# Performance work log

Hardware: AMD Instinct MI355X
Metric: run time of the kernel (lower is better)

Reference implementation:

```python
import jax, jax.numpy as jnp
import numpy as np

B, N, N_IN, MSG_HID, MSG_OUT, N_HID, N_OUT, K = 32, 128, 16, 64, 64, 64, 16, 4
E = N * (N - 1)  # 16256 directed edges, fully connected w/o self-loops


def setup_inputs() -> dict:
    key = jax.random.key(0)
    ks = jax.random.split(key, 8)
    # one-hot relation matrices (NRI convention)
    rows, cols = np.where(np.ones((N, N)) - np.eye(N))
    eye = np.eye(N, dtype=np.float32)
    rel_rec = jnp.asarray(eye[rows])   # [E, N]
    rel_send = jnp.asarray(eye[cols])  # [E, N]
    s = 0.1  # weight init scale
    return {
        "inputs": jax.random.normal(ks[0], (B, N_IN, N), jnp.float32),
        "rel_rec": rel_rec,
        "rel_send": rel_send,
        "rel_types": jax.nn.softmax(jax.random.normal(ks[1], (B, E, K), jnp.float32), axis=-1),
        "W1": jax.random.normal(ks[2], (K, 2 * N_IN, MSG_HID), jnp.float32) * s,
        "b1": jnp.zeros((K, MSG_HID), jnp.float32),
        "W2": jax.random.normal(ks[3], (K, MSG_HID, MSG_OUT), jnp.float32) * s,
        "b2": jnp.zeros((K, MSG_OUT), jnp.float32),
        "Wo1": jax.random.normal(ks[4], (MSG_OUT + N_IN, N_HID), jnp.float32) * s,
        "bo1": jnp.zeros((N_HID,), jnp.float32),
        "Wo2": jax.random.normal(ks[5], (N_HID, N_HID), jnp.float32) * s,
        "bo2": jnp.zeros((N_HID,), jnp.float32),
        "Wo3": jax.random.normal(ks[6], (N_HID, N_OUT), jnp.float32) * s,
        "bo3": jnp.zeros((N_OUT,), jnp.float32),
    }


def reference(inputs, rel_rec, rel_send, rel_types, W1, b1, W2, b2, Wo1, bo1, Wo2, bo2, Wo3, bo3):
    x = jnp.transpose(inputs, (0, 2, 1))                     # [B, N, n_in]
    senders = jnp.einsum('en,bnf->bef', rel_send, x)          # [B, E, n_in]
    receivers = jnp.einsum('en,bnf->bef', rel_rec, x)         # [B, E, n_in]
    pre_msg = jnp.concatenate([senders, receivers], axis=-1)  # [B, E, 2*n_in]
    all_msgs = jnp.zeros((pre_msg.shape[0], pre_msg.shape[1], W2.shape[-1]), pre_msg.dtype)
    for k in range(W1.shape[0]):  # small fixed loop over edge types
        m = jax.nn.relu(pre_msg @ W1[k] + b1[k])
        m = jax.nn.relu(m @ W2[k] + b2[k])
        all_msgs = all_msgs + m * rel_types[:, :, k:k + 1]
    # edge2node aggregation (no normalization in forward path, matches source)
    agg_msgs = jnp.einsum('bem,en->bnm', all_msgs, rel_rec)   # [B, N, msg_out]
    aug_msgs = jnp.concatenate([x, agg_msgs], axis=-1)        # [B, N, n_in+msg_out]
    h = jax.nn.relu(aug_msgs @ Wo1 + bo1)  # dropout disabled (eval mode)
    h = jax.nn.relu(h @ Wo2 + bo2)
    pred = h @ Wo3 + bo3                                      # [B, N, n_out]
    return jnp.transpose(pred, (0, 2, 1))                     # [B, n_out, N]
```

## Files before the change

kernel.cpp:

```cpp
#include <hip/hip_runtime.h>
#include <stdint.h>

#define B_  32
#define N_  128
#define NIN 16
#define K_  4
#define E_  (N_*(N_-1))

typedef float    f4 __attribute__((ext_vector_type(4)));
typedef _Float16 h8 __attribute__((ext_vector_type(8)));
typedef _Float16 h4 __attribute__((ext_vector_type(4)));

__global__ __launch_bounds__(256) void prep(
    const float* __restrict__ inp, const float* __restrict__ W1,
    const float* __restrict__ b1,  const float* __restrict__ W2,
    const float* __restrict__ Wo1, const float* __restrict__ Wo2,
    const float* __restrict__ Wo3, const float* __restrict__ rt,
    _Float16* __restrict__ Sh, _Float16* __restrict__ Rh,
    _Float16* __restrict__ w2h, _Float16* __restrict__ wn,
    _Float16* __restrict__ rtn)
{
    const int bid = blockIdx.x;
    const int tid = threadIdx.x;
    if (bid < 1024) {
        int gid = bid*256 + tid;
        int c0 = (gid & 15)*4;
        int n  = (gid >> 4) & 127;
        int b  = (gid >> 11) & 31;
        int k  = gid >> 16;
        f4 s = {0.f,0.f,0.f,0.f};
        f4 r = *(const f4*)(b1 + k*64 + c0);
        const float* xp  = inp + (b*NIN)*N_ + n;
        const f4* w1s = (const f4*)(W1 + (k*32)*64 + c0);
        const f4* w1r = (const f4*)(W1 + (k*32 + 16)*64 + c0);
        #pragma unroll
        for (int f = 0; f < 16; ++f) {
            float xv = xp[f*N_];
            s += xv * w1s[f*16];
            r += xv * w1r[f*16];
        }
        int base = ((k*B_ + b)*N_ + n)*64 + c0;
        h4 sh, rh;
        #pragma unroll
        for (int u = 0; u < 4; ++u) { sh[u] = (_Float16)s[u]; rh[u] = (_Float16)r[u]; }
        *(h4*)(Sh + base) = sh;
        *(h4*)(Rh + base) = rh;
    } else if (bid < 1088) {
        int t = (bid - 1024)*256 + tid;
        int i    = t & 7;
        int lane = (t >> 3) & 63;
        int nt   = (t >> 9) & 3;
        int ks   = (t >> 11) & 1;
        int k    = t >> 12;
        int c = ks*32 + (lane >> 4)*8 + i;
        int o = nt*16 + (lane & 15);
        w2h[t] = (_Float16)W2[(k*64 + c)*64 + o];
    } else if (bid < 1132) {
        int t = (bid - 1088)*256 + tid;
        int j    = t & 7;
        int lane = (t >> 3) & 63;
        int f    = t >> 9;
        int col = lane & 15, q = lane >> 4, row = q*8 + j;
        float v;
        if (f < 12) {
            int ks = f >> 2, nt = f & 3, i = ks*32 + row;
            v = (i < 80) ? Wo1[i*64 + nt*16 + col] : 0.f;
        } else if (f < 20) {
            int g = f - 12, ks = g >> 2, nt = g & 3, i = ks*32 + row;
            v = Wo2[i*64 + nt*16 + col];
        } else {
            int ks = f - 20, i = ks*32 + row;
            v = Wo3[i*16 + col];
        }
        wn[t] = (_Float16)v;
    } else {
        int t = (bid - 1132)*256 + tid;
        int jg = t & 31;
        int r  = (t >> 5) & 127;
        int b  = t >> 12;
        const f4* rt4p = (const f4*)(rt + (size_t)(b*E_ + r*127)*4);
        #pragma unroll
        for (int u = 0; u < 4; ++u) {
            int j = jg*4 + u;
            if (j < 127) {
                f4 v = rt4p[j];
                int s = j + (j >= r ? 1 : 0);
                #pragma unroll
                for (int k = 0; k < 4; ++k)
                    rtn[((k*B_ + b)*N_ + r)*N_ + s] = (_Float16)v[k];
            } else {
                #pragma unroll
                for (int k = 0; k < 4; ++k)
                    rtn[((k*B_ + b)*N_ + r)*N_ + r] = (_Float16)0.f;
            }
        }
    }
}

__global__ __launch_bounds__(512) void edge_mfma(
    const _Float16* __restrict__ Sh, const _Float16* __restrict__ Rh,
    const _Float16* __restrict__ w2h, const _Float16* __restrict__ rtn,
    const float* __restrict__ b2, float* __restrict__ aggK)
{
    __shared__ _Float16 Ssw[N_*64];
    __shared__ _Float16 Rl[32*64];
    __shared__ _Float16 Rt[32*128];

    const int tid  = threadIdx.x;
    const int wave = tid >> 6;
    const int lane = tid & 63;
    const int col  = lane & 15;
    const int q    = lane >> 4;
    const int bid  = blockIdx.x;
    const int rt4  = bid & 3;
    const int b    = (bid >> 2) & 31;
    const int k    = bid >> 7;
    const int kb   = k*B_ + b;
    const int r0   = rt4*32;

    const _Float16* Sg = Sh + (size_t)kb*(N_*64);
    #pragma unroll
    for (int rnd = 0; rnd < 2; ++rnd) {
        int p  = rnd*512 + tid;
        int s  = p >> 3;
        int c8 = (p & 7) ^ (s & 7);
        *(h8*)(Ssw + p*8) = *(const h8*)(Sg + (s*8 + c8)*8);
    }
    if (tid < 256)
        *(h8*)(Rl + tid*8) = *(const h8*)(Rh + ((size_t)kb*N_ + r0)*64 + tid*8);
    *(h8*)(Rt + tid*8) =
        *(const h8*)(rtn + ((size_t)kb*N_ + r0)*N_ + tid*8);

    const h8* w2v = (const h8*)w2h;
    h8 w2f[2][4];
    #pragma unroll
    for (int ks = 0; ks < 2; ++ks)
        #pragma unroll
        for (int nt = 0; nt < 4; ++nt)
            w2f[ks][nt] = w2v[((k*2 + ks)*4 + nt)*64 + lane];

    f4 b2i[4];
    #pragma unroll
    for (int nt = 0; nt < 4; ++nt) {
        float v = b2[k*64 + nt*16 + col];
        b2i[nt][0] = v; b2i[nt][1] = v; b2i[nt][2] = v; b2i[nt][3] = v;
    }

    __syncthreads();

    const h8 zero8 = {0,0,0,0,0,0,0,0};

    #pragma unroll 1
    for (int rg = 0; rg < 4; ++rg) {
        const int rl = wave*4 + rg;
        const int r  = r0 + rl;
        h8 rf0 = *(const h8*)(Rl + rl*64 + q*8);
        h8 rf1 = *(const h8*)(Rl + rl*64 + (4 + q)*8);
        h4 rth[8];
        #pragma unroll
        for (int mt = 0; mt < 8; ++mt)
            rth[mt] = *(const h4*)(Rt + rl*128 + mt*16 + q*4);

        float aggacc[4] = {0.f, 0.f, 0.f, 0.f};
        #pragma unroll
        for (int mt = 0; mt < 8; ++mt) {
            int s  = mt*16 + col;
            int x0 = (s*8 + (q       ^ (s & 7)))*8;
            int x1 = (s*8 + ((4 + q) ^ (s & 7)))*8;
            h8 a0 = *(const h8*)(Ssw + x0);
            h8 a1 = *(const h8*)(Ssw + x1);
            a0 = __builtin_elementwise_max(a0 + rf0, zero8);
            a1 = __builtin_elementwise_max(a1 + rf1, zero8);
            float rtv[4];
            #pragma unroll
            for (int i = 0; i < 4; ++i) rtv[i] = (float)rth[mt][i];

            #pragma unroll
            for (int nt = 0; nt < 4; ++nt) {
                f4 acc = __builtin_amdgcn_mfma_f32_16x16x32_f16(a0, w2f[0][nt], b2i[nt], 0, 0, 0);
                acc     = __builtin_amdgcn_mfma_f32_16x16x32_f16(a1, w2f[1][nt], acc,    0, 0, 0);
                #pragma unroll
                for (int i = 0; i < 4; ++i)
                    aggacc[nt] += rtv[i] * fmaxf(acc[i], 0.f);
            }
        }
        #pragma unroll
        for (int nt = 0; nt < 4; ++nt) {
            float v = aggacc[nt];
            v += __shfl_xor(v, 16, 64);
            v += __shfl_xor(v, 32, 64);
            if (lane < 16) aggK[((size_t)kb*N_ + r)*64 + nt*16 + lane] = v;
        }
    }
}

__global__ __launch_bounds__(256) void node_mfma(
    const float* __restrict__ aggK, const float* __restrict__ inp,
    const _Float16* __restrict__ wn,
    const float* __restrict__ bo1, const float* __restrict__ bo2,
    const float* __restrict__ bo3, float* __restrict__ out)
{
    __shared__ _Float16 augH[64*128];
    __shared__ _Float16 h12[64*64];

    const int tid = threadIdx.x;
    const int b   = blockIdx.x >> 1;
    const int r0  = (blockIdx.x & 1)*64;

    {
        const int nl = tid >> 2, c4 = tid & 3;
        const int r  = r0 + nl;
        float xv[4];
        #pragma unroll
        for (int u = 0; u < 4; ++u)
            xv[u] = inp[(b*NIN + c4*4 + u)*N_ + r];
        f4 av[4];
        #pragma unroll
        for (int w = 0; w < 4; ++w) {
            int c = w*16 + c4*4;
            f4 a = {0.f,0.f,0.f,0.f};
            #pragma unroll
            for (int k = 0; k < 4; ++k)
                a += *(const f4*)(aggK + (((size_t)k*B_ + b)*N_ + r)*64 + c);
            av[w] = a;
        }
        #pragma unroll
        for (int u = 0; u < 4; ++u) {
            int i = c4*4 + u;
            augH[nl*128 + (((i>>3) ^ (nl&15))<<3) + (i&7)] = (_Float16)xv[u];
        }
        #pragma unroll
        for (int w = 0; w < 4; ++w)
            #pragma unroll
            for (int u = 0; u < 4; ++u) {
                int i = 16 + w*16 + c4*4 + u;
                augH[nl*128 + (((i>>3) ^ (nl&15))<<3) + (i&7)] = (_Float16)av[w][u];
            }
        if (c4 < 2)
            #pragma unroll
            for (int u = 0; u < 8; ++u) {
                int i = 80 + c4*8 + u;
                augH[nl*128 + (((i>>3) ^ (nl&15))<<3) + (i&7)] = (_Float16)0.f;
            }
    }
    __syncthreads();

    const int mt  = tid >> 6, lane = tid & 63;
    const int col = lane & 15, q = lane >> 4;
    const h8* wv   = (const h8*)wn;
    const h8* augV = (const h8*)augH;
    const h8* hv   = (const h8*)h12;
    const int nl   = mt*16 + col;

    f4 acc[4];
    #pragma unroll
    for (int nt = 0; nt < 4; ++nt) {
        float v = bo1[nt*16 + col];
        acc[nt][0] = v; acc[nt][1] = v; acc[nt][2] = v; acc[nt][3] = v;
    }
    #pragma unroll
    for (int ks = 0; ks < 3; ++ks) {
        h8 af = augV[nl*16 + ((ks*4 + q) ^ col)];
        #pragma unroll
        for (int nt = 0; nt < 4; ++nt)
            acc[nt] = __builtin_amdgcn_mfma_f32_16x16x32_f16(af, wv[(ks*4 + nt)*64 + lane], acc[nt], 0, 0, 0);
    }
    #pragma unroll
    for (int nt = 0; nt < 4; ++nt)
        #pragma unroll
        for (int i = 0; i < 4; ++i) {
            int n2 = mt*16 + q*4 + i, o = nt*16 + col;
            h12[n2*64 + (((o>>3) ^ (n2&7))<<3) + (o&7)] = (_Float16)fmaxf(acc[nt][i], 0.f);
        }

    f4 acc2[4];
    #pragma unroll
    for (int nt = 0; nt < 4; ++nt) {
        float v = bo2[nt*16 + col];
        acc2[nt][0] = v; acc2[nt][1] = v; acc2[nt][2] = v; acc2[nt][3] = v;
    }
    #pragma unroll
    for (int ks = 0; ks < 2; ++ks) {
        h8 af = hv[nl*8 + ((ks*4 + q) ^ (col & 7))];
        #pragma unroll
        for (int nt = 0; nt < 4; ++nt)
            acc2[nt] = __builtin_amdgcn_mfma_f32_16x16x32_f16(af, wv[(12 + ks*4 + nt)*64 + lane], acc2[nt], 0, 0, 0);
    }
    #pragma unroll
    for (int nt = 0; nt < 4; ++nt)
        #pragma unroll
        for (int i = 0; i < 4; ++i) {
            int n2 = mt*16 + q*4 + i, o = nt*16 + col;
            h12[n2*64 + (((o>>3) ^ (n2&7))<<3) + (o&7)] = (_Float16)fmaxf(acc2[nt][i], 0.f);
        }

    f4 acc3;
    {
        float v = bo3[col];
        acc3[0] = v; acc3[1] = v; acc3[2] = v; acc3[3] = v;
    }
    #pragma unroll
    for (int ks = 0; ks < 2; ++ks) {
        h8 af = hv[nl*8 + ((ks*4 + q) ^ (col & 7))];
        acc3 = __builtin_amdgcn_mfma_f32_16x16x32_f16(af, wv[(20 + ks)*64 + lane], acc3, 0, 0, 0);
    }
    #pragma unroll
    for (int i = 0; i < 4; ++i) {
        int r = r0 + mt*16 + q*4 + i;
        out[(b*NIN + col)*N_ + r] = acc3[i];
    }
}

extern "C" void kernel_launch(void* const* d_in, const int* in_sizes, int n_in,
                              void* d_out, int out_size, void* d_ws, size_t ws_size,
                              hipStream_t stream)
{
    const float* inp = (const float*)d_in[0];
    const float* rt  = (const float*)d_in[3];
    const float* W1  = (const float*)d_in[4];
    const float* b1  = (const float*)d_in[5];
    const float* W2  = (const float*)d_in[6];
    const float* b2  = (const float*)d_in[7];
    const float* Wo1 = (const float*)d_in[8];
    const float* bo1 = (const float*)d_in[9];
    const float* Wo2 = (const float*)d_in[10];
    const float* bo2 = (const float*)d_in[11];
    const float* Wo3 = (const float*)d_in[12];
    const float* bo3 = (const float*)d_in[13];

    _Float16* Sh   = (_Float16*)d_ws;
    _Float16* Rh   = Sh + (1u << 20);
    _Float16* w2h  = Rh + (1u << 20);
    _Float16* wn   = w2h + 16384;
    _Float16* rtn  = wn + 11264;
    float*    aggK = (float*)(rtn + (1u << 21));

    hipLaunchKernelGGL(prep, dim3(1644), dim3(256), 0, stream,
                       inp, W1, b1, W2, Wo1, Wo2, Wo3, rt, Sh, Rh, w2h, wn, rtn);
    hipLaunchKernelGGL(edge_mfma, dim3(512), dim3(512), 0, stream,
                       Sh, Rh, w2h, rtn, b2, aggK);
    hipLaunchKernelGGL(node_mfma, dim3(64), dim3(256), 0, stream,
                       aggK, inp, wn, bo1, bo2, bo3, (float*)d_out);
}
```

Baseline: 137.7 us.

## Restructure edge kernel: register-resident sender tiles, smaller blocks, fp32 rel_types

The edge kernel now uses 256-thread blocks covering 16 receivers each, giving 1024 blocks. Each wave keeps its half of the sender features in registers rather than staging all senders in swizzled shared memory. The two sender halves are reduced through a shared-memory buffer before one vectorized write to aggK. The rel_types matrix is now stored as fp32 rather than fp16, which drops the conversion but doubles that buffer's write and read traffic. The aggregation uses vector FMAs on the MFMA outputs.

```diff
diff --git a/kernel.cpp b/kernel.cpp
--- a/kernel.cpp
+++ b/kernel.cpp
@@ -18,7 +18,7 @@
     const float* __restrict__ Wo3, const float* __restrict__ rt,
     _Float16* __restrict__ Sh, _Float16* __restrict__ Rh,
     _Float16* __restrict__ w2h, _Float16* __restrict__ wn,
-    _Float16* __restrict__ rtn)
+    float* __restrict__ rtf)
 {
     const int bid = blockIdx.x;
     const int tid = threadIdx.x;
@@ -87,49 +87,54 @@
                 int s = j + (j >= r ? 1 : 0);
                 #pragma unroll
                 for (int k = 0; k < 4; ++k)
-                    rtn[((k*B_ + b)*N_ + r)*N_ + s] = (_Float16)v[k];
+                    rtf[(size_t)((k*B_ + b)*N_ + r)*N_ + s] = v[k];
             } else {
                 #pragma unroll
                 for (int k = 0; k < 4; ++k)
-                    rtn[((k*B_ + b)*N_ + r)*N_ + r] = (_Float16)0.f;
+                    rtf[(size_t)((k*B_ + b)*N_ + r)*N_ + r] = 0.f;
             }
         }
     }
 }
 
-__global__ __launch_bounds__(512) void edge_mfma(
+__global__ __launch_bounds__(256) void edge_mfma(
     const _Float16* __restrict__ Sh, const _Float16* __restrict__ Rh,
-    const _Float16* __restrict__ w2h, const _Float16* __restrict__ rtn,
+    const _Float16* __restrict__ w2h, const float* __restrict__ rtf,
     const float* __restrict__ b2, float* __restrict__ aggK)
 {
-    __shared__ _Float16 Ssw[N_*64];
-    __shared__ _Float16 Rl[32*64];
-    __shared__ _Float16 Rt[32*128];
+    __shared__ _Float16 Rlh[16*64];
+    __shared__ float    Rtf[16*128];
+    __shared__ float    aggW[2][2][8][64];
 
     const int tid  = threadIdx.x;
     const int wave = tid >> 6;
     const int lane = tid & 63;
     const int col  = lane & 15;
     const int q    = lane >> 4;
+    const int h    = wave & 1;
+    const int p    = wave >> 1;
     const int bid  = blockIdx.x;
-    const int rt4  = bid & 3;
-    const int b    = (bid >> 2) & 31;
-    const int k    = bid >> 7;
+    const int re   = bid & 7;
+    const int b    = (bid >> 3) & 31;
+    const int k    = bid >> 8;
     const int kb   = k*B_ + b;
-    const int r0   = rt4*32;
-
-    const _Float16* Sg = Sh + (size_t)kb*(N_*64);
-    #pragma unroll
-    for (int rnd = 0; rnd < 2; ++rnd) {
-        int p  = rnd*512 + tid;
-        int s  = p >> 3;
-        int c8 = (p & 7) ^ (s & 7);
-        *(h8*)(Ssw + p*8) = *(const h8*)(Sg + (s*8 + c8)*8);
-    }
-    if (tid < 256)
-        *(h8*)(Rl + tid*8) = *(const h8*)(Rh + ((size_t)kb*N_ + r0)*64 + tid*8);
-    *(h8*)(Rt + tid*8) =
-        *(const h8*)(rtn + ((size_t)kb*N_ + r0)*N_ + tid*8);
+    const int r0   = re*16;
+
+    if (tid < 128)
+        *(h8*)(Rlh + tid*8) = *(const h8*)(Rh + ((size_t)kb*N_ + r0)*64 + tid*8);
+    {
+        const float* src = rtf + ((size_t)kb*N_ + r0)*N_;
+        *(f4*)(Rtf + tid*4)        = *(const f4*)(src + tid*4);
+        *(f4*)(Rtf + 1024 + tid*4) = *(const f4*)(src + 1024 + tid*4);
+    }
+
+    h8 sf[4][2];
+    const _Float16* Sg = Sh + ((size_t)kb*N_ + h*64)*64;
+    #pragma unroll
+    for (int mt = 0; mt < 4; ++mt) {
+        sf[mt][0] = *(const h8*)(Sg + (mt*16 + col)*64 + q*8);
+        sf[mt][1] = *(const h8*)(Sg + (mt*16 + col)*64 + (4 + q)*8);
+    }
 
     const h8* w2v = (const h8*)w2h;
     h8 w2f[2][4];
@@ -149,48 +154,44 @@
     __syncthreads();
 
     const h8 zero8 = {0,0,0,0,0,0,0,0};
+    const f4 zero4 = {0.f,0.f,0.f,0.f};
 
     #pragma unroll 1
-    for (int rg = 0; rg < 4; ++rg) {
-        const int rl = wave*4 + rg;
-        const int r  = r0 + rl;
-        h8 rf0 = *(const h8*)(Rl + rl*64 + q*8);
-        h8 rf1 = *(const h8*)(Rl + rl*64 + (4 + q)*8);
-        h4 rth[8];
-        #pragma unroll
-        for (int mt = 0; mt < 8; ++mt)
-            rth[mt] = *(const h4*)(Rt + rl*128 + mt*16 + q*4);
-
-        float aggacc[4] = {0.f, 0.f, 0.f, 0.f};
-        #pragma unroll
-        for (int mt = 0; mt < 8; ++mt) {
-            int s  = mt*16 + col;
-            int x0 = (s*8 + (q       ^ (s & 7)))*8;
-            int x1 = (s*8 + ((4 + q) ^ (s & 7)))*8;
-            h8 a0 = *(const h8*)(Ssw + x0);
-            h8 a1 = *(const h8*)(Ssw + x1);
-            a0 = __builtin_elementwise_max(a0 + rf0, zero8);
-            a1 = __builtin_elementwise_max(a1 + rf1, zero8);
-            float rtv[4];
-            #pragma unroll
-            for (int i = 0; i < 4; ++i) rtv[i] = (float)rth[mt][i];
+    for (int rg = 0; rg < 8; ++rg) {
+        const int rl = p*8 + rg;
+        h8 rf0 = *(const h8*)(Rlh + rl*64 + q*8);
+        h8 rf1 = *(const h8*)(Rlh + rl*64 + (4 + q)*8);
+
+        f4 vacc[4] = {zero4, zero4, zero4, zero4};
+        #pragma unroll
+        for (int mt = 0; mt < 4; ++mt) {
+            f4 rt4 = *(const f4*)(Rtf + rl*128 + h*64 + mt*16 + q*4);
+            h8 a0 = __builtin_elementwise_max(sf[mt][0] + rf0, zero8);
+            h8 a1 = __builtin_elementwise_max(sf[mt][1] + rf1, zero8);
 
             #pragma unroll
             for (int nt = 0; nt < 4; ++nt) {
                 f4 acc = __builtin_amdgcn_mfma_f32_16x16x32_f16(a0, w2f[0][nt], b2i[nt], 0, 0, 0);
                 acc     = __builtin_amdgcn_mfma_f32_16x16x32_f16(a1, w2f[1][nt], acc,    0, 0, 0);
-                #pragma unroll
-                for (int i = 0; i < 4; ++i)
-                    aggacc[nt] += rtv[i] * fmaxf(acc[i], 0.f);
+                f4 m = __builtin_elementwise_max(acc, zero4);
+                vacc[nt] += rt4 * m;
             }
         }
         #pragma unroll
         for (int nt = 0; nt < 4; ++nt) {
-            float v = aggacc[nt];
+            float v = vacc[nt][0] + vacc[nt][1] + vacc[nt][2] + vacc[nt][3];
             v += __shfl_xor(v, 16, 64);
             v += __shfl_xor(v, 32, 64);
-            if (lane < 16) aggK[((size_t)kb*N_ + r)*64 + nt*16 + lane] = v;
-        }
+            if (lane < 16) aggW[p][h][rg][nt*16 + lane] = v;
+        }
+    }
+    __syncthreads();
+
+    {
+        int rl = tid >> 4, c4 = tid & 15;
+        f4 v = *(const f4*)(&aggW[rl >> 3][0][rl & 7][c4*4])
+             + *(const f4*)(&aggW[rl >> 3][1][rl & 7][c4*4]);
+        *(f4*)(aggK + ((size_t)kb*N_ + r0 + rl)*64 + c4*4) = v;
     }
 }
 
@@ -332,13 +333,13 @@
     _Float16* Rh   = Sh + (1u << 20);
     _Float16* w2h  = Rh + (1u << 20);
     _Float16* wn   = w2h + 16384;
-    _Float16* rtn  = wn + 11264;
-    float*    aggK = (float*)(rtn + (1u << 21));
+    float*    rtf  = (float*)(wn + 11264);
+    float*    aggK = rtf + (1u << 21);
 
     hipLaunchKernelGGL(prep, dim3(1644), dim3(256), 0, stream,
-                       inp, W1, b1, W2, Wo1, Wo2, Wo3, rt, Sh, Rh, w2h, wn, rtn);
-    hipLaunchKernelGGL(edge_mfma, dim3(512), dim3(512), 0, stream,
-                       Sh, Rh, w2h, rtn, b2, aggK);
+                       inp, W1, b1, W2, Wo1, Wo2, Wo3, rt, Sh, Rh, w2h, wn, rtf);
+    hipLaunchKernelGGL(edge_mfma, dim3(1024), dim3(256), 0, stream,
+                       Sh, Rh, w2h, rtf, b2, aggK);
     hipLaunchKernelGGL(node_mfma, dim3(64), dim3(256), 0, stream,
                        aggK, inp, wn, bo1, bo2, bo3, (float*)d_out);
 }
```

Result: faster. 134.6 us (-2.2%).
